# Kernel optimization log

Measured on AMD Instinct MI355X. Metric: run time of the kernel, lower is better.

## Reference

```python
import jax, jax.numpy as jnp
import numpy as np

BH, W, C, NHEAD = 512, 256, 128, 4
HEAD_DIM = C // NHEAD
EPS = 1e-5


def _xavier(key, shape):
    fan_out, fan_in = shape
    lim = np.sqrt(6.0 / (fan_in + fan_out)).astype(np.float32)
    return jax.random.uniform(key, shape, jnp.float32, -lim, lim)


def setup_inputs() -> dict:
    key = jax.random.key(0)
    ks = jax.random.split(key, 4)
    return {
        "feat_left": jax.random.normal(ks[0], (BH, W, C), jnp.float32),
        "feat_right": jax.random.normal(ks[1], (BH, W, C), jnp.float32),
        "l_proj_weight": _xavier(ks[2], (2 * C, C)),
        "r_proj_weight": _xavier(ks[3], (2 * C, C)),
        "l_proj_bias": jnp.zeros((2 * C,), jnp.float32),
        "r_proj_bias": jnp.zeros((2 * C,), jnp.float32),
        "l_out_weight": _xavier(jax.random.fold_in(key, 10), (C, C)),
        "l_out_bias": jnp.zeros((C,), jnp.float32),
        "r_out_weight": _xavier(jax.random.fold_in(key, 11), (C, C)),
        "r_out_bias": jnp.zeros((C,), jnp.float32),
        "norm_weight": jnp.ones((C,), jnp.float32),
        "norm_bias": jnp.zeros((C,), jnp.float32),
    }


def _layernorm(x, w, b):
    mu = jnp.mean(x, axis=-1, keepdims=True)
    var = jnp.mean(jnp.square(x - mu), axis=-1, keepdims=True)
    return (x - mu) * jax.lax.rsqrt(var + EPS) * w + b


def reference(feat_left, feat_right, l_proj_weight, r_proj_weight,
              l_proj_bias, r_proj_bias, l_out_weight, l_out_bias,
              r_out_weight, r_out_bias, norm_weight, norm_bias):
    bh, w, c = feat_left.shape
    e, hd = NHEAD, HEAD_DIM

    l_n = _layernorm(feat_left, norm_weight, norm_bias)
    r_n = _layernorm(feat_right, norm_weight, norm_bias)

    l_kv = l_n @ l_proj_weight.T + l_proj_bias
    r_kv = r_n @ r_proj_weight.T + r_proj_bias
    l_k, l_v = jnp.split(l_kv, 2, axis=-1)
    r_k, r_v = jnp.split(r_kv, 2, axis=-1)

    l_k = l_k.reshape(bh, w, e, hd)
    r_k = r_k.reshape(bh, w, e, hd)
    l_v = l_v.reshape(bh, w, e, hd)
    r_v = r_v.reshape(bh, w, e, hd)

    # shared score matrix [bh, heads, w_left, w_right]
    attn = jnp.einsum('nwec,nvec->newv', l_k, r_k) * 0.1

    # left attends over right positions (softmax over last axis)
    sm_l = jax.nn.softmax(attn, axis=-1)
    out_l = jnp.einsum('newv,nvec->nwec', sm_l, r_v).reshape(bh, w, c)

    # right attends over left positions (softmax over w axis of same scores)
    sm_r = jax.nn.softmax(attn, axis=2)
    out_r = jnp.einsum('newv,nwec->nvec', sm_r, l_v).reshape(bh, w, c)

    out_l = out_l @ l_out_weight.T + l_out_bias
    out_r = out_r @ r_out_weight.T + r_out_bias

    return feat_left + out_l, feat_right + out_r
```

## Files before the change

kernel.cpp:

```cpp
#include <hip/hip_runtime.h>
#include <hip/hip_bf16.h>

#define BH   512
#define NW   256
#define CC   128
#define TOK  (BH * NW)

typedef __attribute__((ext_vector_type(8))) short short8;
typedef __attribute__((ext_vector_type(4))) float f32x4;
typedef __attribute__((ext_vector_type(4))) int   i32x4;
typedef __attribute__((ext_vector_type(4))) unsigned short us4;
typedef __attribute__((ext_vector_type(2))) unsigned int u32x2;
typedef unsigned short ushort_t;

static __device__ __forceinline__ f32x4 mfma16(short8 a, short8 b, f32x4 c) {
    return __builtin_amdgcn_mfma_f32_16x16x32_bf16(a, b, c, 0, 0, 0);
}

static __device__ __forceinline__ unsigned int pk2(float a, float b) {
    __hip_bfloat162 h = __float22bfloat162_rn(make_float2(a, b));
    return *reinterpret_cast<unsigned int*>(&h);
}
static __device__ __forceinline__ ushort_t f2bf(float f) {
    unsigned int u = __float_as_uint(f);
    u = (u + 0x7fffu + ((u >> 16) & 1u)) >> 16;
    return (ushort_t)u;
}
#if __has_builtin(__builtin_amdgcn_exp2f)
static __device__ __forceinline__ float exp2_fast(float x) { return __builtin_amdgcn_exp2f(x); }
#else
static __device__ __forceinline__ float exp2_fast(float x) { return exp2f(x); }
#endif

__global__ __launch_bounds__(256)
void k_prep(const float* __restrict__ WpL, const float* __restrict__ WpR,
            const float* __restrict__ bpL, const float* __restrict__ bpR,
            const float* __restrict__ WoL, const float* __restrict__ WoR,
            const float* __restrict__ nw,  const float* __restrict__ nb,
            ushort_t* __restrict__ Wb, float* __restrict__ bias2,
            ushort_t* __restrict__ WoB)
{
    if (blockIdx.x < 8) {
        const int gid = blockIdx.x * 256 + threadIdx.x;
        const int row = gid >> 2;
        const int q   = gid & 3;
        const int side = row >> 8;
        const int o    = row & 255;
        const float* Wp = side ? WpR : WpL;
        const float* bp = side ? bpR : bpL;
        const float* wr = Wp + (size_t)o * 128 + q * 32;

        float acc = 0.f;
#pragma unroll
        for (int g = 0; g < 4; ++g) {
            const int c = q * 32 + g * 8;
            float4 wa = *(const float4*)(wr + g * 8);
            float4 wb = *(const float4*)(wr + g * 8 + 4);
            float4 ga = *(const float4*)(nw + c);
            float4 gb = *(const float4*)(nw + c + 4);
            float4 ba = *(const float4*)(nb + c);
            float4 bb = *(const float4*)(nb + c + 4);
            acc += wa.x*ba.x + wa.y*ba.y + wa.z*ba.z + wa.w*ba.w
                 + wb.x*bb.x + wb.y*bb.y + wb.z*bb.z + wb.w*bb.w;
            u32x2 o0, o1;
            o0[0] = pk2(wa.x*ga.x, wa.y*ga.y);
            o0[1] = pk2(wa.z*ga.z, wa.w*ga.w);
            o1[0] = pk2(wb.x*gb.x, wb.y*gb.y);
            o1[1] = pk2(wb.z*gb.z, wb.w*gb.w);
            *(u32x2*)(Wb + (size_t)row * 128 + c)     = o0;
            *(u32x2*)(Wb + (size_t)row * 128 + c + 4) = o1;
        }
        acc += __shfl_xor(acc, 1);
        acc += __shfl_xor(acc, 2);
        if (q == 0) bias2[row] = bp[o] + acc;
    } else {
        const int idx  = (blockIdx.x - 8) * 256 + threadIdx.x;
        const int row2 = idx >> 2;
        const int q    = idx & 3;
        const int side = row2 >> 7;
        const int o    = row2 & 127;
        const float* Wo = side ? WoR : WoL;
        const float* wr = Wo + (size_t)o * 128 + q * 32;
#pragma unroll
        for (int g = 0; g < 4; ++g) {
            float4 wa = *(const float4*)(wr + g * 8);
            float4 wb = *(const float4*)(wr + g * 8 + 4);
            u32x2 o0, o1;
            o0[0] = pk2(wa.x, wa.y); o0[1] = pk2(wa.z, wa.w);
            o1[0] = pk2(wb.x, wb.y); o1[1] = pk2(wb.z, wb.w);
            *(u32x2*)(WoB + (size_t)row2 * 128 + q * 32 + g * 8)     = o0;
            *(u32x2*)(WoB + (size_t)row2 * 128 + q * 32 + g * 8 + 4) = o1;
        }
    }
}

__global__ __launch_bounds__(512)
void k_ln_proj(const float* __restrict__ featL, const float* __restrict__ featR,
               const ushort_t* __restrict__ Wb, const float* __restrict__ bias2,
               ushort_t* __restrict__ kvL,      ushort_t* __restrict__ kvR)
{
    const int side = blockIdx.y;
    const float* feat = side ? featR : featL;
    const ushort_t* W = Wb + side * 32768;
    const float* b2   = bias2 + side * 256;
    ushort_t*    kv   = side ? kvR : kvL;

    const int tile0 = blockIdx.x * 2;
    const int tid = threadIdx.x;
    const int wid = tid >> 6, lane = tid & 63, l16 = lane & 15, lh = lane >> 4;
    const int wn  = wid * 32;

    __shared__ ushort_t Asm[64][136];
    __shared__ ushort_t kvS[64][260];

    const int row = tid >> 3, q = tid & 7;

    float xc[16], xn[16];
    {
        const float* fr = feat + (size_t)(tile0 * 64 + row) * CC + q * 16;
#pragma unroll
        for (int i = 0; i < 4; ++i) {
            float4 v = *(const float4*)(fr + i * 4);
            xc[i*4+0]=v.x; xc[i*4+1]=v.y; xc[i*4+2]=v.z; xc[i*4+3]=v.w;
        }
    }

    short8 Bf[8];
#pragma unroll
    for (int kk = 0; kk < 4; ++kk)
#pragma unroll
        for (int tn = 0; tn < 2; ++tn)
            Bf[kk*2 + tn] = *(const short8*)(W + (size_t)(wn + tn*16 + l16) * CC + kk*32 + lh*8);
    float4 bias[2];
#pragma unroll
    for (int tn = 0; tn < 2; ++tn)
        bias[tn] = *(const float4*)(b2 + wn + tn*16 + lh*4);

    const float kscale = (side == 0 && wn < 128) ? 0.14426950408889634f : 1.0f;

#pragma unroll
    for (int t = 0; t < 2; ++t) {
        const int m0 = (tile0 + t) * 64;

        {
            float s = 0.f, s2 = 0.f;
#pragma unroll
            for (int i = 0; i < 16; ++i) { s += xc[i]; s2 += xc[i]*xc[i]; }
#pragma unroll
            for (int m = 1; m < 8; m <<= 1) { s += __shfl_xor(s, m); s2 += __shfl_xor(s2, m); }
            float mu   = s * (1.f / 128.f);
            float var  = s2 * (1.f / 128.f) - mu * mu;
            float rstd = rsqrtf(var + 1e-5f);
            float a = rstd, bsh = -mu * rstd;
#pragma unroll
            for (int g = 0; g < 2; ++g) {
                i32x4 o;
#pragma unroll
                for (int k = 0; k < 4; ++k)
                    o[k] = (int)pk2(xc[g*8 + 2*k] * a + bsh, xc[g*8 + 2*k + 1] * a + bsh);
                *(i32x4*)&Asm[row][q * 16 + g * 8] = o;
            }
        }
        __syncthreads();

        if (t < 1) {
            const float* fr = feat + (size_t)(m0 + 64 + row) * CC + q * 16;
#pragma unroll
            for (int i = 0; i < 4; ++i) {
                float4 v = *(const float4*)(fr + i * 4);
                xn[i*4+0]=v.x; xn[i*4+1]=v.y; xn[i*4+2]=v.z; xn[i*4+3]=v.w;
            }
        }

        f32x4 acc[4][2];
#pragma unroll
        for (int mt = 0; mt < 4; ++mt)
#pragma unroll
            for (int tn = 0; tn < 2; ++tn)
                acc[mt][tn] = (f32x4){0.f, 0.f, 0.f, 0.f};

#pragma unroll
        for (int kk = 0; kk < 4; ++kk) {
            short8 a[4];
#pragma unroll
            for (int mt = 0; mt < 4; ++mt)
                a[mt] = *(const short8*)&Asm[mt*16 + l16][kk*32 + lh*8];
#pragma unroll
            for (int tn = 0; tn < 2; ++tn)
#pragma unroll
                for (int mt = 0; mt < 4; ++mt)
                    acc[mt][tn] = mfma16(Bf[kk*2 + tn], a[mt], acc[mt][tn]);
        }

#pragma unroll
        for (int mt = 0; mt < 4; ++mt)
#pragma unroll
            for (int tn = 0; tn < 2; ++tn) {
                const int r    = mt*16 + l16;
                const int slot = (wn >> 2) + tn*4 + lh;
                float v0 = (acc[mt][tn][0] + bias[tn].x) * kscale;
                float v1 = (acc[mt][tn][1] + bias[tn].y) * kscale;
                float v2 = (acc[mt][tn][2] + bias[tn].z) * kscale;
                float v3 = (acc[mt][tn][3] + bias[tn].w) * kscale;
                u32x2 wv;
                wv[0] = pk2(v0, v1);
                wv[1] = pk2(v2, v3);
                *(u32x2*)&kvS[r][slot * 4] = wv;
            }
        __syncthreads();

#pragma unroll
        for (int it = 0; it < 8; ++it) {
            int u = it * 512 + tid;
            int r = u >> 6, sl = u & 63;
            u32x2 wv = *(const u32x2*)&kvS[r][sl * 4];
            *(u32x2*)(kv + (size_t)(m0 + r) * 256 + sl * 4) = wv;
        }

        if (t < 1) {
#pragma unroll
            for (int i = 0; i < 16; ++i) xc[i] = xn[i];
        }
    }
}

template<int BF16OUT>
__global__ __launch_bounds__(512, 4)
void k_attn(const ushort_t* __restrict__ kvL, const ushort_t* __restrict__ kvR,
            float* __restrict__ outFBase, ushort_t* __restrict__ outBBase)
{
    const int bx   = blockIdx.x;
    const int work = (bx & 7) * 512 + (bx >> 3);
    const int n    = work >> 3;
    const int e    = (work >> 1) & 3;
    const int dir  = work & 1;
    const ushort_t* kvA = dir ? kvR : kvL;
    const ushort_t* kvB = dir ? kvL : kvR;

    const int tid = threadIdx.x;
    const int wid = tid >> 6, lane = tid & 63, l16 = lane & 15, lh = lane >> 4;
    const int W0 = wid * 32;
    const int kcls = (l16 >> 1) & 3;

    __shared__ ushort_t kB[256][32];
    __shared__ ushort_t vT[32][280];
    __shared__ ushort_t pL[8][32][32];

    {
        const ushort_t* src = kvB + (size_t)n * 256 * 256 + e * 32;
#pragma unroll
        for (int p = 0; p < 2; ++p) {
            int u = tid + p * 512;
            int r = u >> 2, slot = u & 3;
            *(i32x4*)&kB[r][(slot ^ ((r >> 1) & 3)) << 3] =
                *(const i32x4*)(src + (size_t)r * 256 + slot * 8);
        }
    }
    {
        const ushort_t* src = kvB + (size_t)n * 256 * 256 + 128 + e * 32;
#pragma unroll
        for (int u4 = 0; u4 < 4; ++u4) {
            int unit = tid + u4 * 512;
            int cp = unit & 15, vp = unit >> 4;
            unsigned int w0 = *(const unsigned int*)(src + (size_t)(vp*2    ) * 256 + cp*2);
            unsigned int w1 = *(const unsigned int*)(src + (size_t)(vp*2 + 1) * 256 + cp*2);
            *(unsigned int*)&vT[cp*2    ][vp*2] = (w0 & 0xffffu) | (w1 << 16);
            *(unsigned int*)&vT[cp*2 + 1][vp*2] = (w0 >> 16) | (w1 & 0xffff0000u);
        }
    }
    short8 aK[2];
#pragma unroll
    for (int tr = 0; tr < 2; ++tr)
        aK[tr] = *(const short8*)(kvA + (size_t)(n*256 + W0 + tr*16 + l16) * 256 + e*32 + lh*8);

    short8 ones;
#pragma unroll
    for (int i = 0; i < 8; ++i) ones[i] = (short)0x3F80;

    __syncthreads();

    f32x4 oacc[2][2];
#pragma unroll
    for (int tr = 0; tr < 2; ++tr)
#pragma unroll
        for (int ct = 0; ct < 2; ++ct)
            oacc[tr][ct] = (f32x4){0.f, 0.f, 0.f, 0.f};
    f32x4 lacc[2] = {(f32x4){0.f,0.f,0.f,0.f}, (f32x4){0.f,0.f,0.f,0.f}};

#pragma unroll 2
    for (int nc = 0; nc < 8; ++nc) {
        const int vc0 = nc * 32;

        short8 bk0 = *(const short8*)&kB[vc0      + l16][(lh ^ kcls) << 3];
        short8 bk1 = *(const short8*)&kB[vc0 + 16 + l16][(lh ^ kcls) << 3];
        f32x4 s[2][2];
#pragma unroll
        for (int tr = 0; tr < 2; ++tr) {
            s[tr][0] = mfma16(bk0, aK[tr], (f32x4){0.f,0.f,0.f,0.f});
            s[tr][1] = mfma16(bk1, aK[tr], (f32x4){0.f,0.f,0.f,0.f});
        }

#pragma unroll
        for (int tr = 0; tr < 2; ++tr) {
            const int prow = tr*16 + l16;
#pragma unroll
            for (int tc = 0; tc < 2; ++tc) {
                float p0 = exp2_fast(s[tr][tc][0]);
                float p1 = exp2_fast(s[tr][tc][1]);
                float p2 = exp2_fast(s[tr][tc][2]);
                float p3 = exp2_fast(s[tr][tc][3]);
                u32x2 w;
                w[0] = pk2(p0, p1);
                w[1] = pk2(p2, p3);
                const int sL   = 2*tc + (lh >> 1);
                const int pcol = ((sL ^ kcls) << 3) + ((lh & 1) << 2);
                *(u32x2*)&pL[wid][prow][pcol] = w;
            }
        }

        short8 aP[2], bV[2];
#pragma unroll
        for (int tr = 0; tr < 2; ++tr)
            aP[tr] = *(const short8*)&pL[wid][tr*16 + l16][(lh ^ kcls) << 3];
#pragma unroll
        for (int ct = 0; ct < 2; ++ct)
            bV[ct] = *(const short8*)&vT[ct*16 + l16][vc0 + lh*8];
#pragma unroll
        for (int tr = 0; tr < 2; ++tr) {
#pragma unroll
            for (int ct = 0; ct < 2; ++ct)
                oacc[tr][ct] = mfma16(bV[ct], aP[tr], oacc[tr][ct]);
            lacc[tr] = mfma16(ones, aP[tr], lacc[tr]);
        }
    }

#pragma unroll
    for (int tr = 0; tr < 2; ++tr) {
        float rinv = 1.f / lacc[tr][0];
        const int token = n * 256 + W0 + tr*16 + l16;
        if (BF16OUT) {
            ushort_t* outB = outBBase + (size_t)dir * TOK * CC;
#pragma unroll
            for (int ct = 0; ct < 2; ++ct) {
                us4 o;
#pragma unroll
                for (int j = 0; j < 4; ++j)
                    o[j] = f2bf(oacc[tr][ct][j] * rinv);
                *(us4*)(outB + (size_t)token * CC + e*32 + ct*16 + lh*4) = o;
            }
        } else {
            float* outF = outFBase + (size_t)dir * TOK * CC;
#pragma unroll
            for (int ct = 0; ct < 2; ++ct) {
                float4 o;
                o.x = oacc[tr][ct][0] * rinv;
                o.y = oacc[tr][ct][1] * rinv;
                o.z = oacc[tr][ct][2] * rinv;
                o.w = oacc[tr][ct][3] * rinv;
                *(float4*)(outF + (size_t)token * CC + e*32 + ct*16 + lh*4) = o;
            }
        }
    }
}

__global__ __launch_bounds__(512)
void k_outproj_fast(float* __restrict__ outBase, const ushort_t* __restrict__ aoutBase,
                    const float* __restrict__ featL, const float* __restrict__ featR,
                    const ushort_t* __restrict__ WoB,
                    const float* __restrict__ boL, const float* __restrict__ boR)
{
    const int side = blockIdx.y;
    float* io = outBase + (size_t)side * TOK * CC;
    const float* feat = side ? featR : featL;
    const ushort_t* Wo = WoB + side * 16384;
    const float* bo   = side ? boR : boL;
    const ushort_t* src = aoutBase + (size_t)side * TOK * CC;

    const int tile0 = blockIdx.x * 4;
    const int tid = threadIdx.x;
    const int wid = tid >> 6, lane = tid & 63, l16 = lane & 15, lh = lane >> 4;
    const int wm = (wid >> 2) * 32;
    const int wn = (wid & 3) * 32;

    __shared__ ushort_t Asm[2][64][136];

    short8 Bf[8];
#pragma unroll
    for (int kk = 0; kk < 4; ++kk)
#pragma unroll
        for (int tn = 0; tn < 2; ++tn)
            Bf[kk*2 + tn] = *(const short8*)(Wo + (size_t)(wn + tn*16 + l16) * CC + kk*32 + lh*8);
    float4 bias4[2];
#pragma unroll
    for (int nt = 0; nt < 2; ++nt)
        bias4[nt] = *(const float4*)(bo + wn + nt*16 + lh*4);

    i32x4 aReg[2];
#pragma unroll
    for (int i = 0; i < 2; ++i) {
        int u = tid + i * 512;
        int r = u >> 4, c0 = (u & 15) * 8;
        aReg[i] = *(const i32x4*)(src + (size_t)(tile0 * 64 + r) * CC + c0);
    }

#pragma unroll
    for (int t = 0; t < 4; ++t) {
        const int m0 = (tile0 + t) * 64;
        const int p  = t & 1;

#pragma unroll
        for (int i = 0; i < 2; ++i) {
            int u = tid + i * 512;
            int r = u >> 4, c0 = (u & 15) * 8;
            *(i32x4*)&Asm[p][r][c0] = aReg[i];
        }
        __syncthreads();

        if (t < 3) {
#pragma unroll
            for (int i = 0; i < 2; ++i) {
                int u = tid + i * 512;
                int r = u >> 4, c0 = (u & 15) * 8;
                aReg[i] = *(const i32x4*)(src + (size_t)(m0 + 64 + r) * CC + c0);
            }
        }
        float4 ff[2][2];
#pragma unroll
        for (int tr = 0; tr < 2; ++tr)
#pragma unroll
            for (int nt = 0; nt < 2; ++nt)
                ff[tr][nt] = *(const float4*)(feat + (size_t)(m0 + wm + tr*16 + l16) * CC
                                              + wn + nt*16 + lh*4);

        f32x4 acc[2][2];
#pragma unroll
        for (int tr = 0; tr < 2; ++tr)
#pragma unroll
            for (int nt = 0; nt < 2; ++nt)
                acc[tr][nt] = (f32x4){0.f, 0.f, 0.f, 0.f};

#pragma unroll
        for (int kk = 0; kk < 4; ++kk) {
            short8 a[2];
#pragma unroll
            for (int tr = 0; tr < 2; ++tr)
                a[tr] = *(const short8*)&Asm[p][wm + tr*16 + l16][kk*32 + lh*8];
#pragma unroll
            for (int tr = 0; tr < 2; ++tr)
#pragma unroll
                for (int nt = 0; nt < 2; ++nt)
                    acc[tr][nt] = mfma16(Bf[kk*2 + nt], a[tr], acc[tr][nt]);
        }

#pragma unroll
        for (int tr = 0; tr < 2; ++tr) {
            const int token = m0 + wm + tr*16 + l16;
#pragma unroll
            for (int nt = 0; nt < 2; ++nt) {
                const int f0 = wn + nt*16 + lh*4;
                float4 o;
                o.x = acc[tr][nt][0] + bias4[nt].x + ff[tr][nt].x;
                o.y = acc[tr][nt][1] + bias4[nt].y + ff[tr][nt].y;
                o.z = acc[tr][nt][2] + bias4[nt].z + ff[tr][nt].z;
                o.w = acc[tr][nt][3] + bias4[nt].w + ff[tr][nt].w;
                *(float4*)(io + (size_t)token * CC + f0) = o;
            }
        }
    }
}

__global__ __launch_bounds__(512, 4)
void k_outproj_slow(float* __restrict__ outBase,
                    const float* __restrict__ featL, const float* __restrict__ featR,
                    const float* __restrict__ WoL,   const float* __restrict__ WoR,
                    const float* __restrict__ boL,   const float* __restrict__ boR)
{
    const int side = blockIdx.y;
    float* io = outBase + (size_t)side * TOK * CC;
    const float* feat = side ? featR : featL;
    const float* Wo   = side ? WoR   : WoL;
    const float* bo   = side ? boR   : boL;

    const int m0 = blockIdx.x * 64;
    const int tid = threadIdx.x;
    const int wid = tid >> 6, lane = tid & 63, l16 = lane & 15, lh = lane >> 4;
    const int wm = (wid >> 2) * 32;
    const int wn = (wid & 3) * 32;

    __shared__ ushort_t Asm[64][136];
    __shared__ ushort_t Wsm[128][136];

    float4 bias4[2];
#pragma unroll
    for (int nt = 0; nt < 2; ++nt)
        bias4[nt] = *(const float4*)(bo + wn + nt*16 + lh*4);

#pragma unroll
    for (int i = 0; i < 8; ++i) {
        int u = tid + i * 512;
        int r = u >> 5, c4 = (u & 31) * 4;
        float4 w4 = *(const float4*)(Wo + (size_t)r * CC + c4);
        u32x2 wv; wv[0] = pk2(w4.x, w4.y); wv[1] = pk2(w4.z, w4.w);
        *(u32x2*)&Wsm[r][c4] = wv;
    }
#pragma unroll
    for (int i = 0; i < 4; ++i) {
        int u = tid + i * 512;
        int r = u >> 5, c4 = (u & 31) * 4;
        float4 a4 = *(const float4*)(io + (size_t)(m0 + r) * CC + c4);
        u32x2 av; av[0] = pk2(a4.x, a4.y); av[1] = pk2(a4.z, a4.w);
        *(u32x2*)&Asm[r][c4] = av;
    }
    __syncthreads();

    f32x4 acc[2][2];
#pragma unroll
    for (int tr = 0; tr < 2; ++tr)
#pragma unroll
        for (int nt = 0; nt < 2; ++nt)
            acc[tr][nt] = (f32x4){0.f, 0.f, 0.f, 0.f};

#pragma unroll
    for (int kk = 0; kk < 4; ++kk) {
        short8 a[2], b[2];
#pragma unroll
        for (int tr = 0; tr < 2; ++tr)
            a[tr] = *(const short8*)&Asm[wm + tr*16 + l16][kk*32 + lh*8];
#pragma unroll
        for (int nt = 0; nt < 2; ++nt)
            b[nt] = *(const short8*)&Wsm[wn + nt*16 + l16][kk*32 + lh*8];
#pragma unroll
        for (int tr = 0; tr < 2; ++tr)
#pragma unroll
            for (int nt = 0; nt < 2; ++nt)
                acc[tr][nt] = mfma16(b[nt], a[tr], acc[tr][nt]);
    }

#pragma unroll
    for (int tr = 0; tr < 2; ++tr) {
        const int token = m0 + wm + tr*16 + l16;
#pragma unroll
        for (int nt = 0; nt < 2; ++nt) {
            const int f0 = wn + nt*16 + lh*4;
            float4 ff = *(const float4*)(feat + (size_t)token * CC + f0);
            float4 o;
            o.x = acc[tr][nt][0] + bias4[nt].x + ff.x;
            o.y = acc[tr][nt][1] + bias4[nt].y + ff.y;
            o.z = acc[tr][nt][2] + bias4[nt].z + ff.z;
            o.w = acc[tr][nt][3] + bias4[nt].w + ff.w;
            *(float4*)(io + (size_t)token * CC + f0) = o;
        }
    }
}

extern "C" void kernel_launch(void* const* d_in, const int* in_sizes, int n_in,
                              void* d_out, int out_size, void* d_ws, size_t ws_size,
                              hipStream_t stream)
{
    const float* featL = (const float*)d_in[0];
    const float* featR = (const float*)d_in[1];
    const float* WpL   = (const float*)d_in[2];
    const float* WpR   = (const float*)d_in[3];
    const float* bpL   = (const float*)d_in[4];
    const float* bpR   = (const float*)d_in[5];
    const float* WoL   = (const float*)d_in[6];
    const float* boL   = (const float*)d_in[7];
    const float* WoR   = (const float*)d_in[8];
    const float* boR   = (const float*)d_in[9];
    const float* nw    = (const float*)d_in[10];
    const float* nb    = (const float*)d_in[11];

    float* out = (float*)d_out;
    ushort_t* kvL = (ushort_t*)d_ws;
    ushort_t* kvR = kvL + (size_t)TOK * 256;
    ushort_t* aout = kvR + (size_t)TOK * 256;

    const size_t kv_us   = (size_t)TOK * 256 * 2;
    const size_t aout_us = (size_t)TOK * CC * 2;
    const size_t wscr_us = 65536 + 1024 + 32768;
    const bool bf16path = ws_size >= (kv_us + aout_us + wscr_us) * 2;

    if (bf16path) {
        ushort_t* Wb  = aout + aout_us;
        float* bias2  = (float*)(Wb + 65536);
        ushort_t* WoB = (ushort_t*)(bias2 + 512);

        k_prep<<<dim3(12), 256, 0, stream>>>(WpL, WpR, bpL, bpR, WoL, WoR,
                                             nw, nb, Wb, bias2, WoB);
        k_ln_proj<<<dim3(1024, 2), 512, 0, stream>>>(featL, featR, Wb, bias2, kvL, kvR);
        k_attn<1><<<dim3(4096), 512, 0, stream>>>(kvL, kvR, out, aout);
        k_outproj_fast<<<dim3(512, 2), 512, 0, stream>>>(out, aout, featL, featR,
                                                         WoB, boL, boR);
    } else {
        ushort_t* Wb  = (ushort_t*)d_out;
        float* bias2  = (float*)d_out + 32768;
        ushort_t* WoB = (ushort_t*)d_out + 66560;

        k_prep<<<dim3(12), 256, 0, stream>>>(WpL, WpR, bpL, bpR, WoL, WoR,
                                             nw, nb, Wb, bias2, WoB);
        k_ln_proj<<<dim3(1024, 2), 512, 0, stream>>>(featL, featR, Wb, bias2, kvL, kvR);
        k_attn<0><<<dim3(4096), 512, 0, stream>>>(kvL, kvR, out, aout);
        k_outproj_slow<<<dim3(TOK / 64, 2), 512, 0, stream>>>(out, featL, featR,
                                                              WoL, WoR, boL, boR);
    }
}
```

Before: 197.2 us.

## Make LN+projection warp-independent with register A fragments and per-warp staging

The LayerNorm+projection kernel is restructured so each warp loads its own 16-token slices straight into MFMA A-fragment layout. It normalises them in registers and stores its 32-column output slab through a small per-warp shared staging buffer. This removes the block-wide shared A tile and both __syncthreads per tile. In exchange, all eight warps redundantly load and normalise the same input rows, leaning on L1/L2 to absorb the repeated global reads, and output stores become narrower per-warp chunks.

New measurement: 272.4 us. +38.1%, slower.

```diff
diff --git a/kernel.cpp b/kernel.cpp
--- a/kernel.cpp
+++ b/kernel.cpp
@@ -105,25 +105,12 @@
     const float* b2   = bias2 + side * 256;
     ushort_t*    kv   = side ? kvR : kvL;
 
-    const int tile0 = blockIdx.x * 2;
     const int tid = threadIdx.x;
     const int wid = tid >> 6, lane = tid & 63, l16 = lane & 15, lh = lane >> 4;
     const int wn  = wid * 32;
-
-    __shared__ ushort_t Asm[64][136];
-    __shared__ ushort_t kvS[64][260];
-
-    const int row = tid >> 3, q = tid & 7;
-
-    float xc[16], xn[16];
-    {
-        const float* fr = feat + (size_t)(tile0 * 64 + row) * CC + q * 16;
-#pragma unroll
-        for (int i = 0; i < 4; ++i) {
-            float4 v = *(const float4*)(fr + i * 4);
-            xc[i*4+0]=v.x; xc[i*4+1]=v.y; xc[i*4+2]=v.z; xc[i*4+3]=v.w;
-        }
-    }
+    const int tok0 = blockIdx.x * 128;
+
+    __shared__ ushort_t stg[8][16][40];
 
     short8 Bf[8];
 #pragma unroll
@@ -138,88 +125,82 @@
 
     const float kscale = (side == 0 && wn < 128) ? 0.14426950408889634f : 1.0f;
 
-#pragma unroll
-    for (int t = 0; t < 2; ++t) {
-        const int m0 = (tile0 + t) * 64;
+    float xc[32], xn[32];
+    {
+        const float* fr = feat + (size_t)(tok0 + l16) * CC + lh * 8;
+#pragma unroll
+        for (int kk = 0; kk < 4; ++kk) {
+            float4 v0 = *(const float4*)(fr + kk * 32);
+            float4 v1 = *(const float4*)(fr + kk * 32 + 4);
+            xc[kk*8+0]=v0.x; xc[kk*8+1]=v0.y; xc[kk*8+2]=v0.z; xc[kk*8+3]=v0.w;
+            xc[kk*8+4]=v1.x; xc[kk*8+5]=v1.y; xc[kk*8+6]=v1.z; xc[kk*8+7]=v1.w;
+        }
+    }
+
+    for (int t = 0; t < 8; ++t) {
+        const int m0 = tok0 + t * 16;
+
+        float s = 0.f, s2 = 0.f;
+#pragma unroll
+        for (int i = 0; i < 32; ++i) { s += xc[i]; s2 += xc[i]*xc[i]; }
+        s  += __shfl_xor(s, 16);  s  += __shfl_xor(s, 32);
+        s2 += __shfl_xor(s2, 16); s2 += __shfl_xor(s2, 32);
+        float mu   = s * (1.f / 128.f);
+        float var  = s2 * (1.f / 128.f) - mu * mu;
+        float rstd = rsqrtf(var + 1e-5f);
+        float a = rstd, bsh = -mu * rstd;
+
+        short8 afr[4];
+#pragma unroll
+        for (int kk = 0; kk < 4; ++kk) {
+            i32x4 tmp;
+#pragma unroll
+            for (int h = 0; h < 4; ++h)
+                tmp[h] = (int)pk2(xc[kk*8 + 2*h] * a + bsh, xc[kk*8 + 2*h + 1] * a + bsh);
+            afr[kk] = *(short8*)&tmp;
+        }
+
+        if (t < 7) {
+            const float* fr = feat + (size_t)(m0 + 16 + l16) * CC + lh * 8;
+#pragma unroll
+            for (int kk = 0; kk < 4; ++kk) {
+                float4 v0 = *(const float4*)(fr + kk * 32);
+                float4 v1 = *(const float4*)(fr + kk * 32 + 4);
+                xn[kk*8+0]=v0.x; xn[kk*8+1]=v0.y; xn[kk*8+2]=v0.z; xn[kk*8+3]=v0.w;
+                xn[kk*8+4]=v1.x; xn[kk*8+5]=v1.y; xn[kk*8+6]=v1.z; xn[kk*8+7]=v1.w;
+            }
+        }
+
+        f32x4 acc[2];
+        acc[0] = (f32x4){0.f, 0.f, 0.f, 0.f};
+        acc[1] = (f32x4){0.f, 0.f, 0.f, 0.f};
+#pragma unroll
+        for (int kk = 0; kk < 4; ++kk) {
+            acc[0] = mfma16(Bf[kk*2 + 0], afr[kk], acc[0]);
+            acc[1] = mfma16(Bf[kk*2 + 1], afr[kk], acc[1]);
+        }
+
+#pragma unroll
+        for (int tn = 0; tn < 2; ++tn) {
+            float v0 = (acc[tn][0] + bias[tn].x) * kscale;
+            float v1 = (acc[tn][1] + bias[tn].y) * kscale;
+            float v2 = (acc[tn][2] + bias[tn].z) * kscale;
+            float v3 = (acc[tn][3] + bias[tn].w) * kscale;
+            u32x2 wv;
+            wv[0] = pk2(v0, v1);
+            wv[1] = pk2(v2, v3);
+            *(u32x2*)&stg[wid][l16][tn*16 + lh*4] = wv;
+        }
 
         {
-            float s = 0.f, s2 = 0.f;
-#pragma unroll
-            for (int i = 0; i < 16; ++i) { s += xc[i]; s2 += xc[i]*xc[i]; }
-#pragma unroll
-            for (int m = 1; m < 8; m <<= 1) { s += __shfl_xor(s, m); s2 += __shfl_xor(s2, m); }
-            float mu   = s * (1.f / 128.f);
-            float var  = s2 * (1.f / 128.f) - mu * mu;
-            float rstd = rsqrtf(var + 1e-5f);
-            float a = rstd, bsh = -mu * rstd;
-#pragma unroll
-            for (int g = 0; g < 2; ++g) {
-                i32x4 o;
-#pragma unroll
-                for (int k = 0; k < 4; ++k)
-                    o[k] = (int)pk2(xc[g*8 + 2*k] * a + bsh, xc[g*8 + 2*k + 1] * a + bsh);
-                *(i32x4*)&Asm[row][q * 16 + g * 8] = o;
-            }
-        }
-        __syncthreads();
-
-        if (t < 1) {
-            const float* fr = feat + (size_t)(m0 + 64 + row) * CC + q * 16;
-#pragma unroll
-            for (int i = 0; i < 4; ++i) {
-                float4 v = *(const float4*)(fr + i * 4);
-                xn[i*4+0]=v.x; xn[i*4+1]=v.y; xn[i*4+2]=v.z; xn[i*4+3]=v.w;
-            }
-        }
-
-        f32x4 acc[4][2];
-#pragma unroll
-        for (int mt = 0; mt < 4; ++mt)
-#pragma unroll
-            for (int tn = 0; tn < 2; ++tn)
-                acc[mt][tn] = (f32x4){0.f, 0.f, 0.f, 0.f};
-
-#pragma unroll
-        for (int kk = 0; kk < 4; ++kk) {
-            short8 a[4];
-#pragma unroll
-            for (int mt = 0; mt < 4; ++mt)
-                a[mt] = *(const short8*)&Asm[mt*16 + l16][kk*32 + lh*8];
-#pragma unroll
-            for (int tn = 0; tn < 2; ++tn)
-#pragma unroll
-                for (int mt = 0; mt < 4; ++mt)
-                    acc[mt][tn] = mfma16(Bf[kk*2 + tn], a[mt], acc[mt][tn]);
-        }
-
-#pragma unroll
-        for (int mt = 0; mt < 4; ++mt)
-#pragma unroll
-            for (int tn = 0; tn < 2; ++tn) {
-                const int r    = mt*16 + l16;
-                const int slot = (wn >> 2) + tn*4 + lh;
-                float v0 = (acc[mt][tn][0] + bias[tn].x) * kscale;
-                float v1 = (acc[mt][tn][1] + bias[tn].y) * kscale;
-                float v2 = (acc[mt][tn][2] + bias[tn].z) * kscale;
-                float v3 = (acc[mt][tn][3] + bias[tn].w) * kscale;
-                u32x2 wv;
-                wv[0] = pk2(v0, v1);
-                wv[1] = pk2(v2, v3);
-                *(u32x2*)&kvS[r][slot * 4] = wv;
-            }
-        __syncthreads();
-
-#pragma unroll
-        for (int it = 0; it < 8; ++it) {
-            int u = it * 512 + tid;
-            int r = u >> 6, sl = u & 63;
-            u32x2 wv = *(const u32x2*)&kvS[r][sl * 4];
-            *(u32x2*)(kv + (size_t)(m0 + r) * 256 + sl * 4) = wv;
-        }
-
-        if (t < 1) {
-#pragma unroll
-            for (int i = 0; i < 16; ++i) xc[i] = xn[i];
+            const int r = lane >> 2, c0 = (lane & 3) * 8;
+            i32x4 v = *(const i32x4*)&stg[wid][r][c0];
+            *(i32x4*)(kv + (size_t)(m0 + r) * 256 + wn + c0) = v;
+        }
+
+        if (t < 7) {
+#pragma unroll
+            for (int i = 0; i < 32; ++i) xc[i] = xn[i];
         }
     }
 }
```
